# Kernel optimization log

Measured on AMD Instinct MI355X. Metric: run time of the kernel, lower is better.

## Reference

```python
import jax, jax.numpy as jnp
import numpy as np
from jax import lax

B, T, H, E, V = 1000, 101, 256, 256, 64


def _lstm(x, Wih, Whh, bih, bhh):
    # x: [B, T, D_in]; PyTorch gate order i, f, g, o. Initial hidden/cell are zeros.
    Bx = x.shape[0]
    Hh = Whh.shape[1]
    b = bih + bhh
    h0 = jnp.zeros((Bx, Hh), x.dtype)
    c0 = jnp.zeros((Bx, Hh), x.dtype)

    def step(carry, xt):
        h, c = carry
        g = xt @ Wih.T + h @ Whh.T + b  # [B, 4H]
        i, f, gg, o = jnp.split(g, 4, axis=-1)
        c = jax.nn.sigmoid(f) * c + jax.nn.sigmoid(i) * jnp.tanh(gg)
        h = jax.nn.sigmoid(o) * jnp.tanh(c)
        return (h, c), h

    _, hs = lax.scan(step, (h0, c0), jnp.swapaxes(x, 0, 1))  # hs: [T, B, H]
    return jnp.swapaxes(hs, 0, 1)


def setup_inputs():
    key = jax.random.key(0)
    ks = jax.random.split(key, 20)
    n = lambda k, s: jax.random.normal(k, s, jnp.float32) * 0.05
    return {
        'input_ids': jax.random.randint(ks[0], (B, T), 0, V, dtype=jnp.int32),
        'emb': n(ks[1], (V, E)),
        'Wih1': n(ks[2], (4 * H, E)), 'Whh1': n(ks[3], (4 * H, H)),
        'bih1': n(ks[4], (4 * H,)), 'bhh1': n(ks[5], (4 * H,)),
        'Wih2': n(ks[6], (4 * H, H)), 'Whh2': n(ks[7], (4 * H, H)),
        'bih2': n(ks[8], (4 * H,)), 'bhh2': n(ks[9], (4 * H,)),
        'Wattn': n(ks[10], (T, H, H)), 'battn': n(ks[11], (T, H)),
        'W1': n(ks[12], (512, H * T)), 'b1': n(ks[13], (512,)),
        'W2': n(ks[14], (128, 512)), 'b2': n(ks[15], (128,)),
        'W3': n(ks[16], (64, 128)), 'b3': n(ks[17], (64,)),
        'Wout': n(ks[18], (1, 64)), 'bout': n(ks[19], (1,)),
    }


def reference(input_ids, emb, Wih1, Whh1, bih1, bhh1, Wih2, Whh2, bih2, bhh2,
              Wattn, battn, W1, b1, W2, b2, W3, b3, Wout, bout):
    x = emb[input_ids]                                    # [B, T, E]
    h1 = _lstm(x, Wih1, Whh1, bih1, bhh1)                 # [B, T, H]
    h2 = _lstm(h1, Wih2, Whh2, bih2, bhh2)                # [B, T, H]
    # per-timestep Linear (the 101-call loop in torch), fused as one batched GEMM
    attn = jnp.einsum('bth,tkh->btk', h2, Wattn) + battn  # y_t = h_t @ W_t.T + b_t
    w = jax.nn.softmax(attn, axis=2)                      # softmax over feature dim
    applied = w * x                                       # [B, T, E]
    flat = applied.reshape(applied.shape[0], -1)          # [B, T*E]
    d = jax.nn.relu(flat @ W1.T + b1)
    d = jax.nn.relu(d @ W2.T + b2)
    d = jax.nn.relu(d @ W3.T + b3)
    tag = d @ Wout.T + bout                               # [B, 1]
    return tag, applied
```

## Files before the change

kernel.cpp:

```cpp
#include <hip/hip_runtime.h>
#include <hip/hip_bf16.h>


#define B_    1000
#define T_    101
#define E_    256
#define H_    256
#define BPAD  1008
#define MPAD  101824
#define NG    1024
#define NSLICE 63

typedef __bf16 bf16;
typedef __bf16 bf16x8 __attribute__((ext_vector_type(8)));
typedef float  f32x4  __attribute__((ext_vector_type(4)));

__device__ __forceinline__ bf16 f2b(float f){
  unsigned u = __builtin_bit_cast(unsigned, f);
  u += 0x7FFFu + ((u >> 16) & 1u);
  unsigned short h = (unsigned short)(u >> 16);
  return __builtin_bit_cast(bf16, h);
}
__device__ __forceinline__ float b2f(bf16 v){
  unsigned short s = __builtin_bit_cast(unsigned short, v);
  unsigned u = ((unsigned)s) << 16;
  return __builtin_bit_cast(float, u);
}
__device__ __forceinline__ unsigned packbf(float a, float b){
  unsigned ua = __builtin_bit_cast(unsigned, a);
  ua += 0x7FFFu + ((ua >> 16) & 1u);
  unsigned ub = __builtin_bit_cast(unsigned, b);
  ub += 0x7FFFu + ((ub >> 16) & 1u);
  return (ua >> 16) | (ub & 0xffff0000u);
}
__device__ __forceinline__ float sigm(float x){ return 1.f/(1.f + __expf(-x)); }
__device__ __forceinline__ float tanh_(float x){ return 2.f/(1.f + __expf(-2.f*x)) - 1.f; }

__global__ void pack_bT(const float* __restrict__ src, bf16* __restrict__ dst,
                        int N, int K)
{
  const long batch = blockIdx.y;
  src += batch * (long)N * K;
  dst += batch * (long)(K/32) * N * 32;
  const int tid = blockIdx.x * blockDim.x + threadIdx.x;
  const int total = (K/32) * N * 4;
  if (tid >= total) return;
  const int kkc = tid & 3;
  const int rem = tid >> 2;
  const int n = rem % N;
  const int q = rem / N;
  const float* s = src + (long)n*K + q*32 + kkc*8;
  bf16x8 v;
  #pragma unroll
  for (int e=0;e<8;e++) v[e] = f2b(s[e]);
  *reinterpret_cast<bf16x8*>(dst + ((long)q*N + n)*32 + kkc*8) = v;
}

__global__ void tr_f32(const float* __restrict__ src, float* __restrict__ dst,
                       int N, int K)
{
  const int id = blockIdx.x * blockDim.x + threadIdx.x;
  if (id >= N*K) return;
  const int k = id / N, j = id % N;
  dst[(long)k*N + j] = src[(long)j*K + k];
}

__global__ void bias_sum(const float* __restrict__ a, const float* __restrict__ b,
                         float* __restrict__ o, int n)
{
  const int i = blockIdx.x * blockDim.x + threadIdx.x;
  if (i < n) o[i] = a[i] + b[i];
}

__global__ void embed_k(const int* __restrict__ ids, const float* __restrict__ emb,
                        bf16* __restrict__ x)
{
  const int tid = blockIdx.x * blockDim.x + threadIdx.x;
  const int m = tid >> 5;
  const int c = (tid & 31) << 3;
  bf16x8 v;
  if (m < B_*T_) {
    const int id = ids[m];
    const float* e = emb + (long)id*E_ + c;
    #pragma unroll
    for (int j=0;j<8;j++) v[j] = f2b(e[j]);
  } else {
    #pragma unroll
    for (int j=0;j<8;j++) v[j] = f2b(0.f);
  }
  *reinterpret_cast<bf16x8*>(x + (long)m*256 + c) = v;
}

#define MF(a,b,c) __builtin_amdgcn_mfma_f32_16x16x32_bf16((a),(b),(c),0,0,0)
#define LDW(q_,off_)  (*reinterpret_cast<const bf16x8*>(bbW + ((long)(q_)*NG + (off_))*32))
#define LDX8(q_,off_) (*reinterpret_cast<const bf16x8*>(bbX + ((long)(q_)*NG + (off_))*32))

#define XK_ALL() { \
  bf16x8 xA0 = LDX8(0,0), xA1 = LDX8(0,16), xB0, xB1; \
  _Pragma("unroll") \
  for (int h2x=0; h2x<4; ++h2x){ \
    const int q0x = 2*h2x; \
    xB0 = LDX8(q0x+1,0); xB1 = LDX8(q0x+1,16); \
    { bf16x8 ax = *reinterpret_cast<const bf16x8*>(&xbuf[l16*264 + q0x*32 + lg*8]); \
      acc0 = MF(ax,xA0,acc0); acc1 = MF(ax,xA1,acc1); } \
    if (q0x+2 < 8){ xA0 = LDX8(q0x+2,0); xA1 = LDX8(q0x+2,16); } \
    { bf16x8 ax = *reinterpret_cast<const bf16x8*>(&xbuf[l16*264 + (q0x+1)*32 + lg*8]); \
      acc0 = MF(ax,xB0,acc0); acc1 = MF(ax,xB1,acc1); } \
  } }

__launch_bounds__(512, 2)
__global__ void lstm_fused(const bf16* __restrict__ X, const bf16* __restrict__ Wihp,
                           const bf16* __restrict__ Whhp, const float* __restrict__ bias,
                           bf16* __restrict__ Hout, unsigned* __restrict__ hX,
                           unsigned* __restrict__ flags)
{
  __shared__ __align__(16) bf16 hbuf[16*264];
  __shared__ __align__(16) bf16 xbuf[16*264];
  __shared__ float gstage[256*17];
  const int bid = blockIdx.x;
  const int s = bid >> 2, g = bid & 3;
  const int b0 = s * 16;
  const int tid = threadIdx.x;
  const int wave = tid >> 6, lane = tid & 63;
  const int l16 = lane & 15, lg = lane >> 4;
  const int qd  = wave >> 1;
  const int h32 = (wave & 1) * 32;

  const bf16* bbW = Whhp + ((long)(qd*256 + g*64 + h32 + l16) * 32 + lg*8);
  const bf16* bbX = Wihp + ((long)(qd*256 + g*64 + h32 + l16) * 32 + lg*8);

  const int row = tid >> 5;
  const int k32 = tid & 31;
  const int j2  = k32 * 2;
  float c0 = 0.f, c1 = 0.f;

  const long grow = (long)(b0 + row) * T_;
  const bf16* xp  = X    + grow*256 + k32*8;
  bf16*       hop = Hout + grow*256 + g*64 + j2;

  const float bvi0 = bias[      g*64 + j2    ];
  const float bvi1 = bias[      g*64 + j2 + 1];
  const float bvf0 = bias[256 + g*64 + j2    ];
  const float bvf1 = bias[256 + g*64 + j2 + 1];
  const float bvg0 = bias[512 + g*64 + j2    ];
  const float bvg1 = bias[512 + g*64 + j2 + 1];
  const float bvo0 = bias[768 + g*64 + j2    ];
  const float bvo1 = bias[768 + g*64 + j2 + 1];

  unsigned* flag = flags + s*16;
  unsigned* hx0 = hX + (size_t)s*2048 + row*128 + g*32 + k32;
  unsigned* hx1 = hx0 + (size_t)NSLICE*2048;
  const unsigned* rb0 = hX + (size_t)s*2048 + row*128;
  const unsigned* rb1 = rb0 + (size_t)NSLICE*2048;

  const int qo0 = 2*g, qo1 = 2*g + 1;

  for (int i = tid; i < 16*264; i += 512) hbuf[i] = f2b(0.f);
  *reinterpret_cast<bf16x8*>(&xbuf[row*264 + k32*8]) =
      *reinterpret_cast<const bf16x8*>(xp);
  __syncthreads();

  f32x4 acc0 = {0.f,0.f,0.f,0.f}, acc1 = {0.f,0.f,0.f,0.f};
  XK_ALL();
  bf16x8 f0[3], f1[3];
  f0[0] = LDW((qo0+2)&7, 0);  f1[0] = LDW((qo0+2)&7, 16);
  f0[1] = LDW((qo0+3)&7, 0);  f1[1] = LDW((qo0+3)&7, 16);

  for (int t = 0; t < T_; ++t){
    const bf16x8 xreg = *reinterpret_cast<const bf16x8*>(xp + (long)(t+1)*256);

    #pragma unroll
    for (int i = 0; i < 6; ++i){
      if (i < 4){
        const int qn = (qo0 + 4 + i) & 7;
        f0[(i+2)%3] = LDW(qn, 0);
        f1[(i+2)%3] = LDW(qn, 16);
      }
      const int qi = (qo0 + 2 + i) & 7;
      bf16x8 a = *reinterpret_cast<const bf16x8*>(&hbuf[l16*264 + qi*32 + lg*8]);
      acc0 = MF(a, f0[i%3], acc0);
      acc1 = MF(a, f1[i%3], acc1);
    }
    {
      const int jj = wave*32 + l16;
      float* gc0 = &gstage[jj*17 + lg*4];
      gc0[0]=acc0[0]; gc0[1]=acc0[1]; gc0[2]=acc0[2]; gc0[3]=acc0[3];
      float* gc1 = &gstage[(jj+16)*17 + lg*4];
      gc1[0]=acc1[0]; gc1[1]=acc1[1]; gc1[2]=acc1[2]; gc1[3]=acc1[3];
    }
    __syncthreads();

    const float i0 = sigm (bvi0 + gstage[(j2      )*17 + row]);
    const float i1 = sigm (bvi1 + gstage[(j2 +   1)*17 + row]);
    const float f0e= sigm (bvf0 + gstage[(j2 +  64)*17 + row]);
    const float f1e= sigm (bvf1 + gstage[(j2 +  65)*17 + row]);
    const float g0e= tanh_(bvg0 + gstage[(j2 + 128)*17 + row]);
    const float g1e= tanh_(bvg1 + gstage[(j2 + 129)*17 + row]);
    const float o0 = sigm (bvo0 + gstage[(j2 + 192)*17 + row]);
    const float o1 = sigm (bvo1 + gstage[(j2 + 193)*17 + row]);
    c0 = f0e*c0 + i0*g0e;
    c1 = f1e*c1 + i1*g1e;
    const unsigned hw = packbf(o0*tanh_(c0), o1*tanh_(c1));

    *reinterpret_cast<unsigned*>(&hbuf[row*264 + g*64 + j2]) = hw;
    *reinterpret_cast<bf16x8*>(&xbuf[row*264 + k32*8]) = xreg;
    __hip_atomic_store((t&1) ? hx1 : hx0, hw, __ATOMIC_RELAXED, __HIP_MEMORY_SCOPE_AGENT);
    *reinterpret_cast<unsigned*>(hop + (long)t*256) = hw;

    __syncthreads();
    if (tid == 0)
      __hip_atomic_fetch_add(flag, 1u, __ATOMIC_RELAXED, __HIP_MEMORY_SCOPE_AGENT);

    {
      bf16x8 o00 = LDW(qo0, 0), o01 = LDW(qo0, 16);
      bf16x8 o10 = LDW(qo1, 0), o11 = LDW(qo1, 16);
      acc0 = f32x4{0.f,0.f,0.f,0.f};
      acc1 = f32x4{0.f,0.f,0.f,0.f};
      bf16x8 a0 = *reinterpret_cast<const bf16x8*>(&hbuf[l16*264 + qo0*32 + lg*8]);
      acc0 = MF(a0, o00, acc0); acc1 = MF(a0, o01, acc1);
      bf16x8 a1 = *reinterpret_cast<const bf16x8*>(&hbuf[l16*264 + qo1*32 + lg*8]);
      acc0 = MF(a1, o10, acc0); acc1 = MF(a1, o11, acc1);
      XK_ALL();
      f0[0] = LDW((qo0+2)&7, 0);  f1[0] = LDW((qo0+2)&7, 16);
      f0[1] = LDW((qo0+3)&7, 0);  f1[1] = LDW((qo0+3)&7, 16);
    }

    {
      const unsigned tgt = 4u*(t+1);
      if (lane == 0){
        int guard = 0;
        while (__hip_atomic_load(flag, __ATOMIC_RELAXED, __HIP_MEMORY_SCOPE_AGENT) < tgt
               && ++guard < (1<<20))
          __builtin_amdgcn_s_sleep(1);
      }
      asm volatile("" ::: "memory");
      __builtin_amdgcn_sched_barrier(0);
      const unsigned* rb = (t&1) ? rb1 : rb0;
      #pragma unroll
      for (int sb=1; sb<4; ++sb){
        const int g2 = (g + sb) & 3;
        const unsigned w = __hip_atomic_load(rb + g2*32 + k32,
                                             __ATOMIC_RELAXED, __HIP_MEMORY_SCOPE_AGENT);
        *reinterpret_cast<unsigned*>(&hbuf[row*264 + g2*64 + j2]) = w;
      }
    }
    __syncthreads();
  }
}

__launch_bounds__(256)
__global__ void attn_applied(const bf16* __restrict__ H2, const bf16* __restrict__ Wap,
                             const float* __restrict__ battn, const int* __restrict__ ids,
                             const float* __restrict__ emb, float* __restrict__ applied,
                             bf16* __restrict__ flat)
{
  __shared__ __align__(16) bf16 albuf[32*264];
  __shared__ float sbuf[32*257];
  const int mt = blockIdx.x, t = blockIdx.y;
  const int b0 = mt*32;
  const int tid = threadIdx.x;
  const int wave = tid >> 6, lane = tid & 63;
  const int l16 = lane & 15, lg = lane >> 4;

  for (int i = tid; i < 1024; i += 256){
    const int r = i >> 5, cc = (i & 31) << 3;
    const int b = b0 + r;
    bf16x8 v;
    if (b < B_) v = *reinterpret_cast<const bf16x8*>(H2 + ((long)b*T_ + t)*256 + cc);
    else { 
      #pragma unroll
      for (int j=0;j<8;j++) v[j] = f2b(0.f);
    }
    *reinterpret_cast<bf16x8*>(&albuf[r*264 + cc]) = v;
  }
  __syncthreads();

  f32x4 acc[2][4];
  #pragma unroll
  for (int ms=0; ms<2; ++ms)
    #pragma unroll
    for (int ns=0; ns<4; ++ns) acc[ms][ns] = f32x4{0.f,0.f,0.f,0.f};

  const bf16* bb = Wap + (long)t*65536 + ((long)(wave*64 + l16) * 32 + lg*8);
  #pragma unroll 2
  for (int q=0; q<8; ++q){
    bf16x8 a0 = *reinterpret_cast<const bf16x8*>(&albuf[l16*264 + q*32 + lg*8]);
    bf16x8 a1 = *reinterpret_cast<const bf16x8*>(&albuf[(16 + l16)*264 + q*32 + lg*8]);
    #pragma unroll
    for (int ns=0; ns<4; ++ns){
      bf16x8 b = *reinterpret_cast<const bf16x8*>(bb + ((long)q*256 + ns*16) * 32);
      acc[0][ns] = __builtin_amdgcn_mfma_f32_16x16x32_bf16(a0, b, acc[0][ns], 0,0,0);
      acc[1][ns] = __builtin_amdgcn_mfma_f32_16x16x32_bf16(a1, b, acc[1][ns], 0,0,0);
    }
  }
  float bv[4];
  #pragma unroll
  for (int ns=0; ns<4; ++ns) bv[ns] = battn[t*256 + wave*64 + ns*16 + l16];
  #pragma unroll
  for (int ms=0; ms<2; ++ms)
    #pragma unroll
    for (int ns=0; ns<4; ++ns)
      #pragma unroll
      for (int r=0; r<4; ++r)
        sbuf[(ms*16 + lg*4 + r)*257 + wave*64 + ns*16 + l16] = acc[ms][ns][r] + bv[ns];
  __syncthreads();

  const int row = tid >> 3, seg = tid & 7;
  const float* srow = &sbuf[row*257 + seg*32];
  float v[32];
  float mx = -1e30f;
  #pragma unroll
  for (int i=0;i<32;++i){ v[i] = srow[i]; mx = fmaxf(mx, v[i]); }
  #pragma unroll
  for (int off=1; off<8; off<<=1) mx = fmaxf(mx, __shfl_xor(mx, off));
  float s = 0.f;
  #pragma unroll
  for (int i=0;i<32;++i){ v[i] = __expf(v[i] - mx); s += v[i]; }
  #pragma unroll
  for (int off=1; off<8; off<<=1) s += __shfl_xor(s, off);
  const float inv = 1.f / s;
  const int b = b0 + row;
  if (b < B_){
    const int id = ids[b*T_ + t];
    const float* ex = emb + (long)id*256 + seg*32;
    float* ap = applied + ((long)b*T_ + t)*256 + seg*32;
    bf16* fp = flat + (long)b*25856 + t*256 + seg*32;
    #pragma unroll
    for (int i=0;i<32;++i){
      const float val = v[i]*inv*ex[i];
      ap[i] = val;
      fp[i] = f2b(val);
    }
  }
}

__launch_bounds__(512)
__global__ void gemm_mlp1(const bf16* __restrict__ A, const bf16* __restrict__ Bp,
                          float* __restrict__ part)
{
  const int m0 = blockIdx.x * 32;
  const int ks = blockIdx.y;
  const int tid = threadIdx.x;
  const int wave = tid >> 6, lane = tid & 63;
  const int l16 = lane & 15, lg = lane >> 4;
  f32x4 acc[2][4];
  #pragma unroll
  for (int ms=0; ms<2; ++ms)
    #pragma unroll
    for (int ns=0; ns<4; ++ns) acc[ms][ns] = f32x4{0.f,0.f,0.f,0.f};

  const bf16* arow0 = A + (long)(m0 + l16)*25856 + lg*8;
  const bf16* arow1 = A + (long)(m0 + 16 + l16)*25856 + lg*8;
  const bf16* bb = Bp + ((long)(wave*64 + l16) * 32 + lg*8);
  #pragma unroll 2
  for (int q = ks*101; q < ks*101 + 101; ++q){
    bf16x8 a0 = *reinterpret_cast<const bf16x8*>(arow0 + (long)q*32);
    bf16x8 a1 = *reinterpret_cast<const bf16x8*>(arow1 + (long)q*32);
    #pragma unroll
    for (int ns=0; ns<4; ++ns){
      bf16x8 b = *reinterpret_cast<const bf16x8*>(bb + ((long)q*512 + ns*16) * 32);
      acc[0][ns] = __builtin_amdgcn_mfma_f32_16x16x32_bf16(a0, b, acc[0][ns], 0,0,0);
      acc[1][ns] = __builtin_amdgcn_mfma_f32_16x16x32_bf16(a1, b, acc[1][ns], 0,0,0);
    }
  }
  #pragma unroll
  for (int ms=0; ms<2; ++ms)
    #pragma unroll
    for (int ns=0; ns<4; ++ns)
      #pragma unroll
      for (int r=0; r<4; ++r)
        part[((long)ks*1024 + m0 + ms*16 + lg*4 + r)*512 + wave*64 + ns*16 + l16] = acc[ms][ns][r];
}

__global__ void reduce_relu(const float* __restrict__ part, const float* __restrict__ b1,
                            float* __restrict__ d1)
{
  const int idx = blockIdx.x*256 + threadIdx.x;
  const int n = idx & 511, m = idx >> 9;
  float s = b1[n];
  #pragma unroll
  for (int k=0;k<8;k++) s += part[((long)k*1024 + m)*512 + n];
  d1[idx] = fmaxf(s, 0.f);
}

__launch_bounds__(128)
__global__ void mlp_tail(const float* __restrict__ d1, const float* __restrict__ W2T,
                         const float* __restrict__ b2, const float* __restrict__ W3T,
                         const float* __restrict__ b3, const float* __restrict__ Wout,
                         const float* __restrict__ bout, float* __restrict__ tag)
{
  __shared__ float r1[512];
  __shared__ float r2[128];
  __shared__ float r3[64];
  const int b = blockIdx.x;
  const int tid = threadIdx.x;
  for (int i = tid; i < 512; i += 128) r1[i] = d1[(long)b*512 + i];
  __syncthreads();
  float a = b2[tid];
  #pragma unroll 8
  for (int k=0;k<512;++k) a += W2T[k*128 + tid] * r1[k];
  r2[tid] = fmaxf(a, 0.f);
  __syncthreads();
  if (tid < 64){
    float a3 = b3[tid];
    #pragma unroll 8
    for (int k=0;k<128;++k) a3 += W3T[k*64 + tid] * r2[k];
    r3[tid] = fmaxf(a3, 0.f);
  }
  __syncthreads();
  if (tid < 64){
    float p = r3[tid] * Wout[tid];
    #pragma unroll
    for (int off=1; off<64; off<<=1) p += __shfl_xor(p, off);
    if (tid == 0) tag[b] = p + bout[0];
  }
}

extern "C" void kernel_launch(void* const* d_in, const int* in_sizes, int n_in,
                              void* d_out, int out_size, void* d_ws, size_t ws_size,
                              hipStream_t stream)
{
  const int*   ids   = (const int*)  d_in[0];
  const float* emb   = (const float*)d_in[1];
  const float* Wih1  = (const float*)d_in[2];
  const float* Whh1  = (const float*)d_in[3];
  const float* bih1  = (const float*)d_in[4];
  const float* bhh1  = (const float*)d_in[5];
  const float* Wih2  = (const float*)d_in[6];
  const float* Whh2  = (const float*)d_in[7];
  const float* bih2  = (const float*)d_in[8];
  const float* bhh2  = (const float*)d_in[9];
  const float* Wattn = (const float*)d_in[10];
  const float* battn = (const float*)d_in[11];
  const float* W1    = (const float*)d_in[12];
  const float* b1    = (const float*)d_in[13];
  const float* W2    = (const float*)d_in[14];
  const float* b2    = (const float*)d_in[15];
  const float* W3    = (const float*)d_in[16];
  const float* b3    = (const float*)d_in[17];
  const float* Wout  = (const float*)d_in[18];
  const float* bout  = (const float*)d_in[19];
  float* out = (float*)d_out;
  char*  ws  = (char*)d_ws;

  constexpr size_t OW_IH1 = 0;
  constexpr size_t OW_HH1 = 524288;
  constexpr size_t OW_IH2 = 1048576;
  constexpr size_t OW_HH2 = 1572864;
  constexpr size_t OW_ATT = 2097152;
  constexpr size_t OW_W1  = 15335424;
  constexpr size_t OW_W2T = 41811968;
  constexpr size_t OW_W3T = 42074112;
  constexpr size_t OB1    = 42106880;
  constexpr size_t OB2    = 42110976;
  constexpr size_t OXH2   = 42115072;
  constexpr size_t OG     = 94248960;
  constexpr size_t OFLAT  = OG;
  constexpr size_t OPART  = OG + 52953088;
  constexpr size_t OH1    = 302784512;
  constexpr size_t OD1    = 354918400;
  constexpr size_t OHX    = OD1;
  constexpr size_t OFLG   = OD1 + 1032192;
  constexpr size_t NEED   = 357015552;
  if (ws_size < NEED) return;

  bf16*  pIH1 = (bf16*) (ws + OW_IH1);
  bf16*  pHH1 = (bf16*) (ws + OW_HH1);
  bf16*  pIH2 = (bf16*) (ws + OW_IH2);
  bf16*  pHH2 = (bf16*) (ws + OW_HH2);
  bf16*  pATT = (bf16*) (ws + OW_ATT);
  bf16*  pW1  = (bf16*) (ws + OW_W1);
  float* pW2T = (float*)(ws + OW_W2T);
  float* pW3T = (float*)(ws + OW_W3T);
  float* pB1  = (float*)(ws + OB1);
  float* pB2  = (float*)(ws + OB2);
  bf16*  pXH2 = (bf16*) (ws + OXH2);
  bf16*  pFLAT= (bf16*) (ws + OFLAT);
  float* pPART= (float*)(ws + OPART);
  bf16*  pH1  = (bf16*) (ws + OH1);
  float* pD1  = (float*)(ws + OD1);
  unsigned* pHX  = (unsigned*)(ws + OHX);
  unsigned* pFL1 = (unsigned*)(ws + OFLG);
  unsigned* pFL2 = (unsigned*)(ws + OFLG + 4096);

  hipMemsetAsync(ws + OFLG, 0, 8192, stream);

  pack_bT<<<dim3(128),        256, 0, stream>>>(Wih1,  pIH1, 1024, 256);
  pack_bT<<<dim3(128),        256, 0, stream>>>(Whh1,  pHH1, 1024, 256);
  pack_bT<<<dim3(128),        256, 0, stream>>>(Wih2,  pIH2, 1024, 256);
  pack_bT<<<dim3(128),        256, 0, stream>>>(Whh2,  pHH2, 1024, 256);
  pack_bT<<<dim3(32, 101),    256, 0, stream>>>(Wattn, pATT, 256,  256);
  pack_bT<<<dim3(6464),       256, 0, stream>>>(W1,    pW1,  512,  25856);
  tr_f32 <<<dim3(256),        256, 0, stream>>>(W2, pW2T, 128, 512);
  tr_f32 <<<dim3(32),         256, 0, stream>>>(W3, pW3T, 64, 128);
  bias_sum<<<dim3(4),         256, 0, stream>>>(bih1, bhh1, pB1, 1024);
  bias_sum<<<dim3(4),         256, 0, stream>>>(bih2, bhh2, pB2, 1024);

  embed_k<<<dim3(12728), 256, 0, stream>>>(ids, emb, pXH2);

  lstm_fused<<<dim3(252), 512, 0, stream>>>(pXH2, pIH1, pHH1, pB1, pH1,  pHX, pFL1);
  lstm_fused<<<dim3(252), 512, 0, stream>>>(pH1,  pIH2, pHH2, pB2, pXH2, pHX, pFL2);

  hipMemsetAsync(ws + OFLAT + (size_t)B_*25856*2, 0, (size_t)24*25856*2, stream);

  attn_applied<<<dim3(32, 101), 256, 0, stream>>>(pXH2, pATT, battn, ids, emb,
                                                  out + 1000, pFLAT);

  gemm_mlp1  <<<dim3(32, 8), 512, 0, stream>>>(pFLAT, pW1, pPART);
  reduce_relu<<<dim3(2048),  256, 0, stream>>>(pPART, b1, pD1);
  mlp_tail   <<<dim3(1000),  128, 0, stream>>>(pD1, pW2T, b2, pW3T, b3, Wout, bout, out);
}
```

Before: 862.8 us.

## Repartition LSTM across 8 blocks per 32-row batch slice

The persistent LSTM kernel now handles 32 batch rows per slice with each of 8 cooperating blocks owning 32 hidden units, instead of 16 rows split across 4 blocks owning 64 units each. Each weight fragment now feeds two MFMAs over two 16-row halves, and all seven remote recurrent K-chunks are prefetched into registers ahead of the step. The global write of h is moved after the flag increment so it does not delay the signal. The trade-off is more cross-block exchange per step (7 peers instead of 3) and higher register pressure, in exchange for fewer weight loads per row and a grid of 256 blocks. The workspace layout and padding are also adjusted.

```diff
diff --git a/kernel.cpp b/kernel.cpp
--- a/kernel.cpp
+++ b/kernel.cpp
@@ -6,10 +6,9 @@
 #define T_    101
 #define E_    256
 #define H_    256
-#define BPAD  1008
-#define MPAD  101824
 #define NG    1024
-#define NSLICE 63
+#define NSL   32
+#define BPAD2 1024
 
 typedef __bf16 bf16;
 typedef __bf16 bf16x8 __attribute__((ext_vector_type(8)));
@@ -20,11 +19,6 @@
   u += 0x7FFFu + ((u >> 16) & 1u);
   unsigned short h = (unsigned short)(u >> 16);
   return __builtin_bit_cast(bf16, h);
-}
-__device__ __forceinline__ float b2f(bf16 v){
-  unsigned short s = __builtin_bit_cast(unsigned short, v);
-  unsigned u = ((unsigned)s) << 16;
-  return __builtin_bit_cast(float, u);
 }
 __device__ __forceinline__ unsigned packbf(float a, float b){
   unsigned ua = __builtin_bit_cast(unsigned, a);
@@ -92,141 +86,139 @@
 }
 
 #define MF(a,b,c) __builtin_amdgcn_mfma_f32_16x16x32_bf16((a),(b),(c),0,0,0)
-#define LDW(q_,off_)  (*reinterpret_cast<const bf16x8*>(bbW + ((long)(q_)*NG + (off_))*32))
-#define LDX8(q_,off_) (*reinterpret_cast<const bf16x8*>(bbX + ((long)(q_)*NG + (off_))*32))
+#define LDW(q_)  (*reinterpret_cast<const bf16x8*>(bbW + ((long)(q_)*NG)*32))
+#define LDX(q_)  (*reinterpret_cast<const bf16x8*>(bbX + ((long)(q_)*NG)*32))
 
 #define XK_ALL() { \
-  bf16x8 xA0 = LDX8(0,0), xA1 = LDX8(0,16), xB0, xB1; \
+  bf16x8 wxA = LDX(0), wxB; \
   _Pragma("unroll") \
   for (int h2x=0; h2x<4; ++h2x){ \
     const int q0x = 2*h2x; \
-    xB0 = LDX8(q0x+1,0); xB1 = LDX8(q0x+1,16); \
-    { bf16x8 ax = *reinterpret_cast<const bf16x8*>(&xbuf[l16*264 + q0x*32 + lg*8]); \
-      acc0 = MF(ax,xA0,acc0); acc1 = MF(ax,xA1,acc1); } \
-    if (q0x+2 < 8){ xA0 = LDX8(q0x+2,0); xA1 = LDX8(q0x+2,16); } \
-    { bf16x8 ax = *reinterpret_cast<const bf16x8*>(&xbuf[l16*264 + (q0x+1)*32 + lg*8]); \
-      acc0 = MF(ax,xB0,acc0); acc1 = MF(ax,xB1,acc1); } \
+    wxB = LDX(q0x+1); \
+    { bf16x8 aA = *reinterpret_cast<const bf16x8*>(&xbuf[l16*264 + q0x*32 + lg*8]); \
+      bf16x8 aB = *reinterpret_cast<const bf16x8*>(&xbuf[(16+l16)*264 + q0x*32 + lg*8]); \
+      accA = MF(aA,wxA,accA); accB = MF(aB,wxA,accB); } \
+    if (q0x+2 < 8) wxA = LDX(q0x+2); \
+    { bf16x8 aA = *reinterpret_cast<const bf16x8*>(&xbuf[l16*264 + (q0x+1)*32 + lg*8]); \
+      bf16x8 aB = *reinterpret_cast<const bf16x8*>(&xbuf[(16+l16)*264 + (q0x+1)*32 + lg*8]); \
+      accA = MF(aA,wxB,accA); accB = MF(aB,wxB,accB); } \
   } }
 
+#define REMK_PF() { \
+  _Pragma("unroll") \
+  for (int i=0;i<7;++i) fw[i] = LDW((g + 1 + i) & 7); }
+
 __launch_bounds__(512, 2)
-__global__ void lstm_fused(const bf16* __restrict__ X, const bf16* __restrict__ Wihp,
-                           const bf16* __restrict__ Whhp, const float* __restrict__ bias,
-                           bf16* __restrict__ Hout, unsigned* __restrict__ hX,
-                           unsigned* __restrict__ flags)
-{
-  __shared__ __align__(16) bf16 hbuf[16*264];
-  __shared__ __align__(16) bf16 xbuf[16*264];
-  __shared__ float gstage[256*17];
+__global__ void lstm_fused8(const bf16* __restrict__ X, const bf16* __restrict__ Wihp,
+                            const bf16* __restrict__ Whhp, const float* __restrict__ bias,
+                            bf16* __restrict__ Hout, unsigned* __restrict__ hX,
+                            unsigned* __restrict__ flags)
+{
+  __shared__ __align__(16) bf16 hbuf[32*264];
+  __shared__ __align__(16) bf16 xbuf[32*264];
+  __shared__ float gstage[128*33];
   const int bid = blockIdx.x;
-  const int s = bid >> 2, g = bid & 3;
-  const int b0 = s * 16;
+  const int s = bid >> 3, g = bid & 7;
+  const int b0 = s * 32;
   const int tid = threadIdx.x;
   const int wave = tid >> 6, lane = tid & 63;
   const int l16 = lane & 15, lg = lane >> 4;
   const int qd  = wave >> 1;
-  const int h32 = (wave & 1) * 32;
-
-  const bf16* bbW = Whhp + ((long)(qd*256 + g*64 + h32 + l16) * 32 + lg*8);
-  const bf16* bbX = Wihp + ((long)(qd*256 + g*64 + h32 + l16) * 32 + lg*8);
-
-  const int row = tid >> 5;
-  const int k32 = tid & 31;
-  const int j2  = k32 * 2;
+  const int h16 = (wave & 1) * 16;
+
+  const bf16* bbW = Whhp + ((long)(qd*256 + g*32 + h16 + l16) * 32 + lg*8);
+  const bf16* bbX = Wihp + ((long)(qd*256 + g*32 + h16 + l16) * 32 + lg*8);
+
+  const int row = tid >> 4;
+  const int k16 = tid & 15;
+  const int j2  = k16 * 2;
   float c0 = 0.f, c1 = 0.f;
 
   const long grow = (long)(b0 + row) * T_;
-  const bf16* xp  = X    + grow*256 + k32*8;
-  bf16*       hop = Hout + grow*256 + g*64 + j2;
-
-  const float bvi0 = bias[      g*64 + j2    ];
-  const float bvi1 = bias[      g*64 + j2 + 1];
-  const float bvf0 = bias[256 + g*64 + j2    ];
-  const float bvf1 = bias[256 + g*64 + j2 + 1];
-  const float bvg0 = bias[512 + g*64 + j2    ];
-  const float bvg1 = bias[512 + g*64 + j2 + 1];
-  const float bvo0 = bias[768 + g*64 + j2    ];
-  const float bvo1 = bias[768 + g*64 + j2 + 1];
+  const bf16* xp  = X    + grow*256 + k16*16;
+  bf16*       hop = Hout + grow*256 + g*32 + j2;
+
+  const float bvi0 = bias[      g*32 + j2    ];
+  const float bvi1 = bias[      g*32 + j2 + 1];
+  const float bvf0 = bias[256 + g*32 + j2    ];
+  const float bvf1 = bias[256 + g*32 + j2 + 1];
+  const float bvg0 = bias[512 + g*32 + j2    ];
+  const float bvg1 = bias[512 + g*32 + j2 + 1];
+  const float bvo0 = bias[768 + g*32 + j2    ];
+  const float bvo1 = bias[768 + g*32 + j2 + 1];
 
   unsigned* flag = flags + s*16;
-  unsigned* hx0 = hX + (size_t)s*2048 + row*128 + g*32 + k32;
-  unsigned* hx1 = hx0 + (size_t)NSLICE*2048;
-  const unsigned* rb0 = hX + (size_t)s*2048 + row*128;
-  const unsigned* rb1 = rb0 + (size_t)NSLICE*2048;
-
-  const int qo0 = 2*g, qo1 = 2*g + 1;
-
-  for (int i = tid; i < 16*264; i += 512) hbuf[i] = f2b(0.f);
-  *reinterpret_cast<bf16x8*>(&xbuf[row*264 + k32*8]) =
-      *reinterpret_cast<const bf16x8*>(xp);
+  unsigned* hx0 = hX + (size_t)s*4096 + row*128 + g*16 + k16;
+  unsigned* hx1 = hx0 + (size_t)NSL*4096;
+  const unsigned* rb0 = hX + (size_t)s*4096 + row*128;
+  const unsigned* rb1 = rb0 + (size_t)NSL*4096;
+
+  for (int i = tid; i < 32*264; i += 512) hbuf[i] = f2b(0.f);
+  *reinterpret_cast<bf16x8*>(&xbuf[row*264 + k16*16])     = *reinterpret_cast<const bf16x8*>(xp);
+  *reinterpret_cast<bf16x8*>(&xbuf[row*264 + k16*16 + 8]) = *reinterpret_cast<const bf16x8*>(xp + 8);
   __syncthreads();
 
-  f32x4 acc0 = {0.f,0.f,0.f,0.f}, acc1 = {0.f,0.f,0.f,0.f};
+  f32x4 accA = {0.f,0.f,0.f,0.f}, accB = {0.f,0.f,0.f,0.f};
   XK_ALL();
-  bf16x8 f0[3], f1[3];
-  f0[0] = LDW((qo0+2)&7, 0);  f1[0] = LDW((qo0+2)&7, 16);
-  f0[1] = LDW((qo0+3)&7, 0);  f1[1] = LDW((qo0+3)&7, 16);
+  bf16x8 fw[7];
+  REMK_PF();
 
   for (int t = 0; t < T_; ++t){
-    const bf16x8 xreg = *reinterpret_cast<const bf16x8*>(xp + (long)(t+1)*256);
-
-    #pragma unroll
-    for (int i = 0; i < 6; ++i){
-      if (i < 4){
-        const int qn = (qo0 + 4 + i) & 7;
-        f0[(i+2)%3] = LDW(qn, 0);
-        f1[(i+2)%3] = LDW(qn, 16);
-      }
-      const int qi = (qo0 + 2 + i) & 7;
-      bf16x8 a = *reinterpret_cast<const bf16x8*>(&hbuf[l16*264 + qi*32 + lg*8]);
-      acc0 = MF(a, f0[i%3], acc0);
-      acc1 = MF(a, f1[i%3], acc1);
+    const bf16x8 xrA = *reinterpret_cast<const bf16x8*>(xp + (long)(t+1)*256);
+    const bf16x8 xrB = *reinterpret_cast<const bf16x8*>(xp + (long)(t+1)*256 + 8);
+
+    #pragma unroll
+    for (int i = 0; i < 7; ++i){
+      const int qi = (g + 1 + i) & 7;
+      bf16x8 aA = *reinterpret_cast<const bf16x8*>(&hbuf[l16*264 + qi*32 + lg*8]);
+      bf16x8 aB = *reinterpret_cast<const bf16x8*>(&hbuf[(16+l16)*264 + qi*32 + lg*8]);
+      accA = MF(aA, fw[i], accA);
+      accB = MF(aB, fw[i], accB);
     }
     {
-      const int jj = wave*32 + l16;
-      float* gc0 = &gstage[jj*17 + lg*4];
-      gc0[0]=acc0[0]; gc0[1]=acc0[1]; gc0[2]=acc0[2]; gc0[3]=acc0[3];
-      float* gc1 = &gstage[(jj+16)*17 + lg*4];
-      gc1[0]=acc1[0]; gc1[1]=acc1[1]; gc1[2]=acc1[2]; gc1[3]=acc1[3];
+      const int jj = wave*16 + l16;
+      float* gc = &gstage[jj*33 + lg*4];
+      gc[0]=accA[0]; gc[1]=accA[1]; gc[2]=accA[2]; gc[3]=accA[3];
+      gc[16]=accB[0]; gc[17]=accB[1]; gc[18]=accB[2]; gc[19]=accB[3];
     }
     __syncthreads();
 
-    const float i0 = sigm (bvi0 + gstage[(j2      )*17 + row]);
-    const float i1 = sigm (bvi1 + gstage[(j2 +   1)*17 + row]);
-    const float f0e= sigm (bvf0 + gstage[(j2 +  64)*17 + row]);
-    const float f1e= sigm (bvf1 + gstage[(j2 +  65)*17 + row]);
-    const float g0e= tanh_(bvg0 + gstage[(j2 + 128)*17 + row]);
-    const float g1e= tanh_(bvg1 + gstage[(j2 + 129)*17 + row]);
-    const float o0 = sigm (bvo0 + gstage[(j2 + 192)*17 + row]);
-    const float o1 = sigm (bvo1 + gstage[(j2 + 193)*17 + row]);
+    const float i0 = sigm (bvi0 + gstage[(j2     )*33 + row]);
+    const float i1 = sigm (bvi1 + gstage[(j2 +  1)*33 + row]);
+    const float f0e= sigm (bvf0 + gstage[(j2 + 32)*33 + row]);
+    const float f1e= sigm (bvf1 + gstage[(j2 + 33)*33 + row]);
+    const float g0e= tanh_(bvg0 + gstage[(j2 + 64)*33 + row]);
+    const float g1e= tanh_(bvg1 + gstage[(j2 + 65)*33 + row]);
+    const float o0 = sigm (bvo0 + gstage[(j2 + 96)*33 + row]);
+    const float o1 = sigm (bvo1 + gstage[(j2 + 97)*33 + row]);
     c0 = f0e*c0 + i0*g0e;
     c1 = f1e*c1 + i1*g1e;
     const unsigned hw = packbf(o0*tanh_(c0), o1*tanh_(c1));
 
-    *reinterpret_cast<unsigned*>(&hbuf[row*264 + g*64 + j2]) = hw;
-    *reinterpret_cast<bf16x8*>(&xbuf[row*264 + k32*8]) = xreg;
+    *reinterpret_cast<unsigned*>(&hbuf[row*264 + g*32 + j2]) = hw;
+    *reinterpret_cast<bf16x8*>(&xbuf[row*264 + k16*16])     = xrA;
+    *reinterpret_cast<bf16x8*>(&xbuf[row*264 + k16*16 + 8]) = xrB;
     __hip_atomic_store((t&1) ? hx1 : hx0, hw, __ATOMIC_RELAXED, __HIP_MEMORY_SCOPE_AGENT);
-    *reinterpret_cast<unsigned*>(hop + (long)t*256) = hw;
 
     __syncthreads();
     if (tid == 0)
       __hip_atomic_fetch_add(flag, 1u, __ATOMIC_RELAXED, __HIP_MEMORY_SCOPE_AGENT);
 
+    *reinterpret_cast<unsigned*>(hop + (long)t*256) = hw;
+
     {
-      bf16x8 o00 = LDW(qo0, 0), o01 = LDW(qo0, 16);
-      bf16x8 o10 = LDW(qo1, 0), o11 = LDW(qo1, 16);
-      acc0 = f32x4{0.f,0.f,0.f,0.f};
-      acc1 = f32x4{0.f,0.f,0.f,0.f};
-      bf16x8 a0 = *reinterpret_cast<const bf16x8*>(&hbuf[l16*264 + qo0*32 + lg*8]);
-      acc0 = MF(a0, o00, acc0); acc1 = MF(a0, o01, acc1);
-      bf16x8 a1 = *reinterpret_cast<const bf16x8*>(&hbuf[l16*264 + qo1*32 + lg*8]);
-      acc0 = MF(a1, o10, acc0); acc1 = MF(a1, o11, acc1);
+      bf16x8 wo = LDW(g);
+      accA = f32x4{0.f,0.f,0.f,0.f};
+      accB = f32x4{0.f,0.f,0.f,0.f};
+      bf16x8 aA = *reinterpret_cast<const bf16x8*>(&hbuf[l16*264 + g*32 + lg*8]);
+      bf16x8 aB = *reinterpret_cast<const bf16x8*>(&hbuf[(16+l16)*264 + g*32 + lg*8]);
+      accA = MF(aA, wo, accA); accB = MF(aB, wo, accB);
       XK_ALL();
-      f0[0] = LDW((qo0+2)&7, 0);  f1[0] = LDW((qo0+2)&7, 16);
-      f0[1] = LDW((qo0+3)&7, 0);  f1[1] = LDW((qo0+3)&7, 16);
+      REMK_PF();
     }
 
     {
-      const unsigned tgt = 4u*(t+1);
+      const unsigned tgt = 8u*(t+1);
       if (lane == 0){
         int guard = 0;
         while (__hip_atomic_load(flag, __ATOMIC_RELAXED, __HIP_MEMORY_SCOPE_AGENT) < tgt
@@ -237,11 +229,11 @@
       __builtin_amdgcn_sched_barrier(0);
       const unsigned* rb = (t&1) ? rb1 : rb0;
       #pragma unroll
-      for (int sb=1; sb<4; ++sb){
-        const int g2 = (g + sb) & 3;
-        const unsigned w = __hip_atomic_load(rb + g2*32 + k32,
+      for (int sb=1; sb<8; ++sb){
+        const int g2 = (g + sb) & 7;
+        const unsigned w = __hip_atomic_load(rb + row*128 + g2*16 + k16,
                                              __ATOMIC_RELAXED, __HIP_MEMORY_SCOPE_AGENT);
-        *reinterpret_cast<unsigned*>(&hbuf[row*264 + g2*64 + j2]) = w;
+        *reinterpret_cast<unsigned*>(&hbuf[row*264 + g2*32 + j2]) = w;
       }
     }
     __syncthreads();
@@ -454,14 +446,13 @@
   constexpr size_t OB1    = 42106880;
   constexpr size_t OB2    = 42110976;
   constexpr size_t OXH2   = 42115072;
-  constexpr size_t OG     = 94248960;
-  constexpr size_t OFLAT  = OG;
-  constexpr size_t OPART  = OG + 52953088;
-  constexpr size_t OH1    = 302784512;
-  constexpr size_t OD1    = 354918400;
-  constexpr size_t OHX    = OD1;
-  constexpr size_t OFLG   = OD1 + 1032192;
-  constexpr size_t NEED   = 357015552;
+  constexpr size_t OH1    = 95069184;
+  constexpr size_t OFLAT  = 148023296;
+  constexpr size_t OPART  = 200976384;
+  constexpr size_t OD1    = 217753600;
+  constexpr size_t OHX    = 219850752;
+  constexpr size_t OFLG   = 220899328;
+  constexpr size_t NEED   = 220907520;
   if (ws_size < NEED) return;
 
   bf16*  pIH1 = (bf16*) (ws + OW_IH1);
@@ -475,15 +466,16 @@
   float* pB1  = (float*)(ws + OB1);
   float* pB2  = (float*)(ws + OB2);
   bf16*  pXH2 = (bf16*) (ws + OXH2);
+  bf16*  pH1  = (bf16*) (ws + OH1);
   bf16*  pFLAT= (bf16*) (ws + OFLAT);
   float* pPART= (float*)(ws + OPART);
-  bf16*  pH1  = (bf16*) (ws + OH1);
   float* pD1  = (float*)(ws + OD1);
   unsigned* pHX  = (unsigned*)(ws + OHX);
   unsigned* pFL1 = (unsigned*)(ws + OFLG);
   unsigned* pFL2 = (unsigned*)(ws + OFLG + 4096);
 
   hipMemsetAsync(ws + OFLG, 0, 8192, stream);
+  hipMemsetAsync(ws + OFLAT + (size_t)B_*25856*2, 0, (size_t)24*25856*2, stream);
 
   pack_bT<<<dim3(128),        256, 0, stream>>>(Wih1,  pIH1, 1024, 256);
   pack_bT<<<dim3(128),        256, 0, stream>>>(Whh1,  pHH1, 1024, 256);
@@ -496,12 +488,10 @@
   bias_sum<<<dim3(4),         256, 0, stream>>>(bih1, bhh1, pB1, 1024);
   bias_sum<<<dim3(4),         256, 0, stream>>>(bih2, bhh2, pB2, 1024);
 
-  embed_k<<<dim3(12728), 256, 0, stream>>>(ids, emb, pXH2);
-
-  lstm_fused<<<dim3(252), 512, 0, stream>>>(pXH2, pIH1, pHH1, pB1, pH1,  pHX, pFL1);
-  lstm_fused<<<dim3(252), 512, 0, stream>>>(pH1,  pIH2, pHH2, pB2, pXH2, pHX, pFL2);
-
-  hipMemsetAsync(ws + OFLAT + (size_t)B_*25856*2, 0, (size_t)24*25856*2, stream);
+  embed_k<<<dim3(12928), 256, 0, stream>>>(ids, emb, pXH2);
+
+  lstm_fused8<<<dim3(256), 512, 0, stream>>>(pXH2, pIH1, pHH1, pB1, pH1,  pHX, pFL1);
+  lstm_fused8<<<dim3(256), 512, 0, stream>>>(pH1,  pIH2, pHH2, pB2, pXH2, pHX, pFL2);
 
   attn_applied<<<dim3(32, 101), 256, 0, stream>>>(pXH2, pATT, battn, ids, emb,
                                                   out + 1000, pFLAT);
```

New measurement: 1.092 ms. 26.5% more time.

## Keep six recurrent weight slices resident in LDS across LSTM timesteps

Applied to the files above, without the earlier changes.

Each LSTM block now loads six of its eight recurrent-weight K-slices into a 120 KB LDS buffer once before the time loop. Each step then reads those slices from LDS instead of streaming them from global memory/L2 through a register rotation. The per-step hidden-state store to global is moved after the barrier and flag increment, and the padding memset is issued before the LSTMs. The larger LDS footprint limits occupancy to one block per CU, which the 252-block persistent grid still fits.

```diff
diff --git a/kernel.cpp b/kernel.cpp
--- a/kernel.cpp
+++ b/kernel.cpp
@@ -20,11 +20,6 @@
   u += 0x7FFFu + ((u >> 16) & 1u);
   unsigned short h = (unsigned short)(u >> 16);
   return __builtin_bit_cast(bf16, h);
-}
-__device__ __forceinline__ float b2f(bf16 v){
-  unsigned short s = __builtin_bit_cast(unsigned short, v);
-  unsigned u = ((unsigned)s) << 16;
-  return __builtin_bit_cast(float, u);
 }
 __device__ __forceinline__ unsigned packbf(float a, float b){
   unsigned ua = __builtin_bit_cast(unsigned, a);
@@ -109,11 +104,12 @@
   } }
 
 __launch_bounds__(512, 2)
-__global__ void lstm_fused(const bf16* __restrict__ X, const bf16* __restrict__ Wihp,
-                           const bf16* __restrict__ Whhp, const float* __restrict__ bias,
-                           bf16* __restrict__ Hout, unsigned* __restrict__ hX,
-                           unsigned* __restrict__ flags)
-{
+__global__ void lstm_v3(const bf16* __restrict__ X, const bf16* __restrict__ Wihp,
+                        const bf16* __restrict__ Whhp, const float* __restrict__ bias,
+                        bf16* __restrict__ Hout, unsigned* __restrict__ hX,
+                        unsigned* __restrict__ flags)
+{
+  __shared__ __align__(16) bf16 wlds[6*256*40];
   __shared__ __align__(16) bf16 hbuf[16*264];
   __shared__ __align__(16) bf16 xbuf[16*264];
   __shared__ float gstage[256*17];
@@ -158,28 +154,37 @@
   for (int i = tid; i < 16*264; i += 512) hbuf[i] = f2b(0.f);
   *reinterpret_cast<bf16x8*>(&xbuf[row*264 + k32*8]) =
       *reinterpret_cast<const bf16x8*>(xp);
+  #pragma unroll
+  for (int it = 0; it < 12; ++it){
+    const int f = tid + it*512;
+    const int qloc = f >> 10;
+    const int rem  = f & 1023;
+    const int lcol = rem >> 2;
+    const int lgw  = rem & 3;
+    const int qdw  = lcol >> 6, jw = lcol & 63;
+    const int gcol = qdw*256 + g*64 + jw;
+    const int qglob = (qo0 + 2 + qloc) & 7;
+    *reinterpret_cast<bf16x8*>(&wlds[(qloc*256 + lcol)*40 + lgw*8]) =
+      *reinterpret_cast<const bf16x8*>(Whhp + ((long)qglob*NG + gcol)*32 + lgw*8);
+  }
   __syncthreads();
 
   f32x4 acc0 = {0.f,0.f,0.f,0.f}, acc1 = {0.f,0.f,0.f,0.f};
   XK_ALL();
-  bf16x8 f0[3], f1[3];
-  f0[0] = LDW((qo0+2)&7, 0);  f1[0] = LDW((qo0+2)&7, 16);
-  f0[1] = LDW((qo0+3)&7, 0);  f1[1] = LDW((qo0+3)&7, 16);
+
+  const int lc0 = qd*64 + h32 + l16;
 
   for (int t = 0; t < T_; ++t){
     const bf16x8 xreg = *reinterpret_cast<const bf16x8*>(xp + (long)(t+1)*256);
 
     #pragma unroll
     for (int i = 0; i < 6; ++i){
-      if (i < 4){
-        const int qn = (qo0 + 4 + i) & 7;
-        f0[(i+2)%3] = LDW(qn, 0);
-        f1[(i+2)%3] = LDW(qn, 16);
-      }
       const int qi = (qo0 + 2 + i) & 7;
-      bf16x8 a = *reinterpret_cast<const bf16x8*>(&hbuf[l16*264 + qi*32 + lg*8]);
-      acc0 = MF(a, f0[i%3], acc0);
-      acc1 = MF(a, f1[i%3], acc1);
+      bf16x8 a  = *reinterpret_cast<const bf16x8*>(&hbuf[l16*264 + qi*32 + lg*8]);
+      bf16x8 w0 = *reinterpret_cast<const bf16x8*>(&wlds[(i*256 + lc0     )*40 + lg*8]);
+      bf16x8 w1 = *reinterpret_cast<const bf16x8*>(&wlds[(i*256 + lc0 + 16)*40 + lg*8]);
+      acc0 = MF(a, w0, acc0);
+      acc1 = MF(a, w1, acc1);
     }
     {
       const int jj = wave*32 + l16;
@@ -205,11 +210,12 @@
     *reinterpret_cast<unsigned*>(&hbuf[row*264 + g*64 + j2]) = hw;
     *reinterpret_cast<bf16x8*>(&xbuf[row*264 + k32*8]) = xreg;
     __hip_atomic_store((t&1) ? hx1 : hx0, hw, __ATOMIC_RELAXED, __HIP_MEMORY_SCOPE_AGENT);
-    *reinterpret_cast<unsigned*>(hop + (long)t*256) = hw;
 
     __syncthreads();
     if (tid == 0)
       __hip_atomic_fetch_add(flag, 1u, __ATOMIC_RELAXED, __HIP_MEMORY_SCOPE_AGENT);
+
+    *reinterpret_cast<unsigned*>(hop + (long)t*256) = hw;
 
     {
       bf16x8 o00 = LDW(qo0, 0), o01 = LDW(qo0, 16);
@@ -221,8 +227,6 @@
       bf16x8 a1 = *reinterpret_cast<const bf16x8*>(&hbuf[l16*264 + qo1*32 + lg*8]);
       acc0 = MF(a1, o10, acc0); acc1 = MF(a1, o11, acc1);
       XK_ALL();
-      f0[0] = LDW((qo0+2)&7, 0);  f1[0] = LDW((qo0+2)&7, 16);
-      f0[1] = LDW((qo0+3)&7, 0);  f1[1] = LDW((qo0+3)&7, 16);
     }
 
     {
@@ -484,6 +488,7 @@
   unsigned* pFL2 = (unsigned*)(ws + OFLG + 4096);
 
   hipMemsetAsync(ws + OFLG, 0, 8192, stream);
+  hipMemsetAsync(ws + OFLAT + (size_t)B_*25856*2, 0, (size_t)24*25856*2, stream);
 
   pack_bT<<<dim3(128),        256, 0, stream>>>(Wih1,  pIH1, 1024, 256);
   pack_bT<<<dim3(128),        256, 0, stream>>>(Whh1,  pHH1, 1024, 256);
@@ -498,10 +503,8 @@
 
   embed_k<<<dim3(12728), 256, 0, stream>>>(ids, emb, pXH2);
 
-  lstm_fused<<<dim3(252), 512, 0, stream>>>(pXH2, pIH1, pHH1, pB1, pH1,  pHX, pFL1);
-  lstm_fused<<<dim3(252), 512, 0, stream>>>(pH1,  pIH2, pHH2, pB2, pXH2, pHX, pFL2);
-
-  hipMemsetAsync(ws + OFLAT + (size_t)B_*25856*2, 0, (size_t)24*25856*2, stream);
+  lstm_v3<<<dim3(252), 512, 0, stream>>>(pXH2, pIH1, pHH1, pB1, pH1,  pHX, pFL1);
+  lstm_v3<<<dim3(252), 512, 0, stream>>>(pH1,  pIH2, pHH2, pB2, pXH2, pHX, pFL2);
 
   attn_applied<<<dim3(32, 101), 256, 0, stream>>>(pXH2, pATT, battn, ids, emb,
                                                   out + 1000, pFLAT);
```

New measurement: 930.6 us. 7.9% more time.
